# Kernel optimization log

Hardware: AMD Instinct MI355X
Metric: run time of the kernel (lower is better)

The kernel has to match this reference:

```python
import jax, jax.numpy as jnp
import numpy as np

B, S, D, H, L, K = 16, 384, 512, 8, 4, 7
HD = D // H
MAXLEN = 400


def _pos_encoding(d=D, max_len=MAXLEN):
    # Faithful to the (unusual) torch loop: even idx i -> sin(pos/10000**(2i/d)),
    # odd idx i+1 -> cos(pos/10000**(2(i+1)/d))
    pe = np.zeros((max_len, d), dtype=np.float32)
    pos = np.arange(max_len, dtype=np.float64)[:, None]
    i = np.arange(0, d, 2)
    pe[:, i] = np.sin(pos / 10000.0 ** (2 * i / d))
    pe[:, i + 1] = np.cos(pos / 10000.0 ** (2 * (i + 1) / d))
    return jnp.asarray(pe)

POS_ENC = _pos_encoding()


def layer_norm(x, g, b, eps=1e-5):
    m = jnp.mean(x, -1, keepdims=True)
    v = jnp.mean((x - m) ** 2, -1, keepdims=True)
    return (x - m) * jax.lax.rsqrt(v + eps) * g + b


def dsconv(x, dw_w, pw_w, pw_b):
    # x: [B,S,D]; depthwise conv1d (no bias) then pointwise 1x1 (bias)
    xc = jnp.transpose(x, (0, 2, 1))  # [B,D,S]
    y = jax.lax.conv_general_dilated(
        xc, dw_w, window_strides=(1,), padding=[(K // 2, K // 2)],
        dimension_numbers=("NCH", "OIH", "NCH"), feature_group_count=D)  # [B,D,S]
    return jnp.einsum("bcs,oc->bso", y, pw_w) + pw_b  # [B,S,D]


def setup_inputs():
    key = jax.random.key(0)
    ks = jax.random.split(key, 16)
    sc = 0.02
    inp = {
        "x": jax.random.normal(ks[0], (B, S, D), jnp.float32),
        "mask": jax.random.randint(ks[1], (B, S), 0, 2, jnp.int32),
        "dw_w": jax.random.normal(ks[2], (L, D, 1, K), jnp.float32) * sc,
        "pw_w": jax.random.normal(ks[3], (L, D, D), jnp.float32) * sc,
        "pw_b": jnp.zeros((L, D), jnp.float32),
        "conv_ln_g": jnp.ones((L, D), jnp.float32),
        "conv_ln_b": jnp.zeros((L, D), jnp.float32),
        "pos_ln_g": jnp.ones((D,), jnp.float32),
        "pos_ln_b": jnp.zeros((D,), jnp.float32),
        "wq": jax.random.normal(ks[4], (D, D), jnp.float32) * sc,
        "bq": jnp.zeros((D,), jnp.float32),
        "wk": jax.random.normal(ks[5], (D, D), jnp.float32) * sc,
        "bk": jnp.zeros((D,), jnp.float32),
        "wv": jax.random.normal(ks[6], (D, D), jnp.float32) * sc,
        "bv": jnp.zeros((D,), jnp.float32),
        "wo": jax.random.normal(ks[7], (D, D), jnp.float32) * sc,
        "bo": jnp.zeros((D,), jnp.float32),
        "ff_ln_g": jnp.ones((D,), jnp.float32),
        "ff_ln_b": jnp.zeros((D,), jnp.float32),
        "ff_w": jax.random.normal(ks[8], (D, D), jnp.float32) * sc,
        "ff_b": jnp.zeros((D,), jnp.float32),
    }
    return inp


def attention(x, mask, wq, bq, wk, bk, wv, bv, wo, bo):
    def heads(w, b):
        y = jnp.einsum("bsd,od->bso", x, w) + b
        return jnp.transpose(y.reshape(B, S, H, HD), (0, 2, 1, 3))  # [B,H,S,HD]
    q, k, v = heads(wq, bq), heads(wk, bk), heads(wv, bv)
    energy = jnp.einsum("bhqd,bhkd->bhqk", q, k) / jnp.sqrt(jnp.float32(HD))
    m = (mask == 1)[:, None, None, :]  # [B,1,1,S]
    energy = jnp.where(m, jnp.float32(-1e10), energy)
    alpha = jax.nn.softmax(energy, axis=-1)  # dropout = identity (eval)
    a = jnp.einsum("bhqk,bhkd->bhqd", alpha, v)
    a = jnp.transpose(a, (0, 2, 1, 3)).reshape(B, S, D)
    return jnp.einsum("bsd,od->bso", a, wo) + bo


def reference(x, mask, dw_w, pw_w, pw_b, conv_ln_g, conv_ln_b, pos_ln_g, pos_ln_b,
              wq, bq, wk, bk, wv, bv, wo, bo, ff_ln_g, ff_ln_b, ff_w, ff_b):
    out = x + POS_ENC[None, :S, :]
    res = out
    out = layer_norm(out, pos_ln_g, pos_ln_b)
    for i in range(L):
        out = jax.nn.relu(dsconv(out, dw_w[i], pw_w[i], pw_b[i]))
        out = out + res  # dropout = identity (eval)
        res = out
        out = layer_norm(out, conv_ln_g[i], conv_ln_b[i])
    out = attention(out, mask, wq, bq, wk, bk, wv, bv, wo, bo)
    out = out + res
    res = out
    out = layer_norm(out, ff_ln_g, ff_ln_b)
    out = jax.nn.relu(jnp.einsum("bsd,od->bso", out, ff_w) + ff_b)
    return out + res
```

## Files before the change

kernel.cpp:

```cpp
#include <hip/hip_runtime.h>

#define BB 16
#define SS 384
#define DD 512
#define HH 8
#define HDIM 64
#define LLAY 4
#define KW 7
#define MM (BB*SS)

typedef unsigned short u16;
typedef unsigned int u32;
typedef short short8v __attribute__((ext_vector_type(8)));
typedef float floatx4 __attribute__((ext_vector_type(4)));

__device__ __forceinline__ float bf2f(u16 u) {
    union { u32 i; float f; } v; v.i = ((u32)u) << 16; return v.f;
}
__device__ __forceinline__ u16 f2bf(float f) {
    union { float f; u32 i; } v; v.f = f;
    return (u16)((v.i + 0x7FFFu + ((v.i >> 16) & 1u)) >> 16);
}
__device__ __forceinline__ bool sniff_f32(const void* dtp) {
    return *((const u32*)dtp) == 0x3F800000u;
}
__device__ __forceinline__ float ldf(const void* p, long i, bool f32) {
    return f32 ? ((const float*)p)[i] : bf2f(((const u16*)p)[i]);
}
__device__ __forceinline__ short8v ldfrag_scalar(const void* p, long i, bool f32) {
    short8v r;
    if (f32) {
        const float* q = (const float*)p + i;
#pragma unroll
        for (int j = 0; j < 8; j++) r[j] = (short)f2bf(q[j]);
    } else {
        r = *(const short8v*)((const u16*)p + i);
    }
    return r;
}

__device__ __forceinline__ void load_lds16(const u16* g, u16* l) {
    __builtin_amdgcn_global_load_lds((const __attribute__((address_space(1))) void*)g,
                                     (__attribute__((address_space(3))) void*)l, 16, 0, 0);
}
__device__ __forceinline__ int swz(int row) { return (row & 3) ^ ((row >> 2) & 3); }
__device__ __forceinline__ short8v lds_frag(const u16* buf, int row, int quad) {
    return *(const short8v*)(buf + ((size_t)row * 4 + (quad ^ swz(row))) * 8);
}

#define WCV_DW 2359296
#define WCV_TOT (WCV_DW + LLAY*KW*DD)
#define NCVB ((WCV_TOT + 255) / 256)

__global__ __launch_bounds__(256) void posln_cvt_kernel(
    const void* __restrict__ x, const void* __restrict__ g, const void* __restrict__ bvec,
    u16* __restrict__ res, u16* __restrict__ out,
    const void* __restrict__ pw_w, const void* __restrict__ wq,
    const void* __restrict__ wk, const void* __restrict__ wv,
    const void* __restrict__ wo, const void* __restrict__ ff_w,
    const void* __restrict__ dw_w, u16* __restrict__ wdst,
    const void* __restrict__ dtp) {
    const bool f32 = sniff_f32(dtp);
    const int tid = threadIdx.x;
    if (blockIdx.x >= MM) {
        const int i = (blockIdx.x - MM) * 256 + tid;
        if (i >= WCV_TOT) return;
        const void* src; long idx;
        if (i < 1048576) { src = pw_w; idx = i; }
        else if (i < WCV_DW) {
            const int j = i - 1048576;
            const int m = j >> 18;
            idx = j & 262143;
            src = (m == 0) ? wq : (m == 1) ? wk : (m == 2) ? wv : (m == 3) ? wo : ff_w;
        } else {
            const int j = i - WCV_DW;
            const int l = j / (KW * DD);
            const int r1 = j % (KW * DD);
            const int t = r1 / DD, c = r1 % DD;
            src = dw_w; idx = ((long)l * DD + c) * KW + t;
        }
        wdst[i] = f2bf(ldf(src, idx, f32));
        return;
    }
    const int row = blockIdx.x;
    const int s = row % SS;
    float v[2];
#pragma unroll
    for (int i = 0; i < 2; i++) {
        const int d = tid + i * 256;
        const float freq = __expf(-(float)d * 0.035977892078032f);
        const float arg = (float)s * freq;
        const float pe = (d & 1) ? __cosf(arg) : __sinf(arg);
        v[i] = ldf(x, (long)row * DD + d, f32) + pe;
        res[row * DD + d] = f2bf(v[i]);
    }
    float sum = v[0] + v[1], sq = v[0] * v[0] + v[1] * v[1];
#pragma unroll
    for (int off = 32; off; off >>= 1) { sum += __shfl_down(sum, off); sq += __shfl_down(sq, off); }
    __shared__ float red[4][2];
    const int wv2 = tid >> 6;
    if ((tid & 63) == 0) { red[wv2][0] = sum; red[wv2][1] = sq; }
    __syncthreads();
    sum = red[0][0] + red[1][0] + red[2][0] + red[3][0];
    sq  = red[0][1] + red[1][1] + red[2][1] + red[3][1];
    const float mean = sum * (1.f / DD);
    const float rstd = rsqrtf(sq * (1.f / DD) - mean * mean + 1e-5f);
#pragma unroll
    for (int i = 0; i < 2; i++) {
        const int d = tid + i * 256;
        out[row * DD + d] = f2bf((v[i] - mean) * rstd * ldf(g, d, f32) + ldf(bvec, d, f32));
    }
}

template <int VEC>
__global__ __launch_bounds__(256) void dwconv_kernel(const u16* __restrict__ in,
                                                     const void* __restrict__ w, int layer,
                                                     u16* __restrict__ out,
                                                     const void* __restrict__ dtp) {
    if constexpr (VEC) {
        const int bsw = (blockIdx.x & 7) * (MM * DD / 8 / 256 / 8) + (blockIdx.x >> 3);
        const int idx = bsw * 256 + threadIdx.x;
        const int c8 = (idx & 63) * 8;
        const int ms = idx >> 6;
        const int s = ms % SS;
        const u16* wl = (const u16*)w + (size_t)layer * KW * DD;
        float acc[8] = {0, 0, 0, 0, 0, 0, 0, 0};
#pragma unroll
        for (int t = 0; t < KW; t++) {
            const int ss2 = s + t - 3;
            if (ss2 >= 0 && ss2 < SS) {
                const short8v iv = *(const short8v*)(in + (size_t)(ms + t - 3) * DD + c8);
                const short8v wv = *(const short8v*)(wl + t * DD + c8);
#pragma unroll
                for (int j = 0; j < 8; j++)
                    acc[j] += bf2f((u16)iv[j]) * bf2f((u16)wv[j]);
            }
        }
        short8v ov;
#pragma unroll
        for (int j = 0; j < 8; j++) ov[j] = (short)f2bf(acc[j]);
        *(short8v*)(out + (size_t)ms * DD + c8) = ov;
    } else {
        const bool f32 = sniff_f32(dtp);
        const long woff = (long)layer * DD * KW;
        const int idx = blockIdx.x * 256 + threadIdx.x;
        const int c = idx & (DD - 1);
        const int ms = idx >> 9;
        const int s = ms % SS;
        float acc = 0.f;
#pragma unroll
        for (int t = 0; t < KW; t++) {
            const int ss2 = s + t - 3;
            if (ss2 >= 0 && ss2 < SS)
                acc += bf2f(in[(ms + t - 3) * DD + c]) * ldf(w, woff + c * KW + t, f32);
        }
        out[idx] = f2bf(acc);
    }
}

__device__ __forceinline__ void stage_tile16(const u16* A, const u16* W, int m0,
                                             u16* Abuf, u16* Wbuf, int tid, int k0) {
#pragma unroll
    for (int j = 0; j < 4; j++) {
        const int c = j * 512 + tid;
        const int row = c >> 2;
        const int kpart = (c & 3) ^ swz(row);
        load_lds16(W + (size_t)row * DD + k0 + kpart * 8, Wbuf + (size_t)c * 8);
    }
    if (tid < 64) {
        const int row = tid >> 2;
        const int kpart = (tid & 3) ^ swz(row);
        load_lds16(A + (size_t)(m0 + row) * DD + k0 + kpart * 8, Abuf + (size_t)tid * 8);
    }
}

__device__ __forceinline__ void kloop16(const u16* A, const u16* W, int m0,
                                        u16* Abuf, u16* Wbuf,
                                        int tid, int wave, int ln15, int quad,
                                        floatx4 acc[4]) {
    stage_tile16(A, W, m0, Abuf, Wbuf, tid, 0);
    __syncthreads();
    for (int ks = 0; ks < 16; ks++) {
        const int cur = ks & 1;
        u16* Ab = Abuf + cur * (16 * 32);
        u16* Wb = Wbuf + cur * (DD * 32);
        if (ks < 15)
            stage_tile16(A, W, m0, Abuf + (cur ^ 1) * (16 * 32),
                         Wbuf + (cur ^ 1) * (DD * 32), tid, (ks + 1) * 32);
        const short8v a0 = lds_frag(Ab, ln15, quad);
#pragma unroll
        for (int nt = 0; nt < 4; nt++) {
            const short8v b = lds_frag(Wb, wave * 64 + nt * 16 + ln15, quad);
            acc[nt] = __builtin_amdgcn_mfma_f32_16x16x32_bf16(a0, b, acc[nt], 0, 0, 0);
        }
        __syncthreads();
    }
}

template <int RELU, int DO_LN, int FINAL, int WVEC>
__global__ __launch_bounds__(512, 4) void gemm16_kernel(
    const u16* __restrict__ A, const void* __restrict__ W, int wlayer,
    const void* __restrict__ bias, const void* __restrict__ g,
    const void* __restrict__ bvec, int blayer,
    const u16* __restrict__ res_in, u16* __restrict__ res_out,
    void* __restrict__ out, const void* __restrict__ dtp) {
    const bool f32 = sniff_f32(dtp);
    const long woff = (long)wlayer * DD * DD;
    const long voff = (long)blayer * DD;
    __shared__ float part[8][16][2];
    __shared__ __align__(16) u16 Wbuf[2 * DD * 32];
    __shared__ __align__(16) u16 Abuf[2 * 16 * 32];
    const int tid = threadIdx.x;
    const int m0 = blockIdx.x * 16;
    const int wave = tid >> 6, lane = tid & 63;
    const int ln15 = lane & 15, quad = lane >> 4;

    floatx4 acc[4];
#pragma unroll
    for (int nt = 0; nt < 4; nt++) acc[nt] = {0.f, 0.f, 0.f, 0.f};

    if constexpr (WVEC) {
        kloop16(A, (const u16*)W + woff, m0, Abuf, Wbuf, tid, wave, ln15, quad, acc);
    } else {
        const u16* A0 = A + (size_t)(m0 + ln15) * DD + quad * 8;
#pragma unroll
        for (int ks = 0; ks < 16; ks++) {
            const int k0 = ks * 32;
            short8v a0 = *(const short8v*)(A0 + k0);
            short8v b[4];
#pragma unroll
            for (int nt = 0; nt < 4; nt++) {
                const long wrow = woff + (long)(wave * 64 + nt * 16 + ln15) * DD + quad * 8 + k0;
                b[nt] = ldfrag_scalar(W, wrow, f32);
            }
#pragma unroll
            for (int nt = 0; nt < 4; nt++)
                acc[nt] = __builtin_amdgcn_mfma_f32_16x16x32_bf16(a0, b[nt], acc[nt], 0, 0, 0);
        }
    }

#pragma unroll
    for (int nt = 0; nt < 4; nt++) {
        const int col = wave * 64 + nt * 16 + ln15;
        const float bval = ldf(bias, voff + col, f32);
#pragma unroll
        for (int r = 0; r < 4; r++) {
            const int m = m0 + quad * 4 + r;
            float y = acc[nt][r] + bval;
            if (RELU) y = fmaxf(y, 0.f);
            y += bf2f(res_in[(size_t)m * DD + col]);
            if (res_out) res_out[(size_t)m * DD + col] = f2bf(y);
            acc[nt][r] = y;
        }
    }
    if constexpr (DO_LN) {
        float ls[4], lq[4];
#pragma unroll
        for (int r = 0; r < 4; r++) {
            float s = 0.f, q = 0.f;
#pragma unroll
            for (int nt = 0; nt < 4; nt++) { const float y = acc[nt][r]; s += y; q += y * y; }
            ls[r] = s; lq[r] = q;
        }
#pragma unroll
        for (int off = 1; off < 16; off <<= 1)
#pragma unroll
            for (int r = 0; r < 4; r++) {
                ls[r] += __shfl_xor(ls[r], off);
                lq[r] += __shfl_xor(lq[r], off);
            }
        if (ln15 == 0) {
#pragma unroll
            for (int r = 0; r < 4; r++) {
                part[wave][quad * 4 + r][0] = ls[r];
                part[wave][quad * 4 + r][1] = lq[r];
            }
        }
        __syncthreads();
        float mean[4], rstd[4];
#pragma unroll
        for (int r = 0; r < 4; r++) {
            const int rr = quad * 4 + r;
            float s = 0.f, q = 0.f;
#pragma unroll
            for (int wv = 0; wv < 8; wv++) { s += part[wv][rr][0]; q += part[wv][rr][1]; }
            const float mn = s * (1.f / DD);
            mean[r] = mn;
            rstd[r] = rsqrtf(q * (1.f / DD) - mn * mn + 1e-5f);
        }
#pragma unroll
        for (int nt = 0; nt < 4; nt++) {
            const int col = wave * 64 + nt * 16 + ln15;
            const float gv = ldf(g, voff + col, f32);
            const float bv = ldf(bvec, voff + col, f32);
#pragma unroll
            for (int r = 0; r < 4; r++) {
                const int m = m0 + quad * 4 + r;
                ((u16*)out)[(size_t)m * DD + col] =
                    f2bf((acc[nt][r] - mean[r]) * rstd[r] * gv + bv);
            }
        }
    } else {
#pragma unroll
        for (int nt = 0; nt < 4; nt++) {
            const int col = wave * 64 + nt * 16 + ln15;
#pragma unroll
            for (int r = 0; r < 4; r++) {
                const int m = m0 + quad * 4 + r;
                if (FINAL && f32) ((float*)out)[(size_t)m * DD + col] = acc[nt][r];
                else              ((u16*)out)[(size_t)m * DD + col] = f2bf(acc[nt][r]);
            }
        }
    }
}

#define VPAD 40
template <int WVEC>
__global__ __launch_bounds__(512, 4) void qkv16_kernel(
    const u16* __restrict__ A,
    const void* __restrict__ Wq, const void* __restrict__ Wk, const void* __restrict__ Wv,
    const void* __restrict__ bq, const void* __restrict__ bk, const void* __restrict__ bv,
    u16* __restrict__ qo, u16* __restrict__ ko, u16* __restrict__ vo,
    const void* __restrict__ dtp) {
    const bool f32 = sniff_f32(dtp);
    const int sel = blockIdx.y;
    const void* W = (sel == 0) ? Wq : (sel == 1) ? Wk : Wv;
    const void* bias = (sel == 0) ? bq : (sel == 1) ? bk : bv;
    u16* out = (sel == 0) ? qo : (sel == 1) ? ko : vo;

    __shared__ __align__(16) u16 Wbuf[2 * DD * 32];
    __shared__ __align__(16) u16 Abuf[2 * 16 * 32];
    u16 (*vtile)[64][VPAD] = (u16 (*)[64][VPAD])Wbuf;

    const int tid = threadIdx.x;
    const int m0 = blockIdx.x * 16;
    const int wave = tid >> 6, lane = tid & 63;
    const int ln15 = lane & 15, quad = lane >> 4;
    const int bidx = m0 / SS;

    floatx4 acc[4];
#pragma unroll
    for (int nt = 0; nt < 4; nt++) acc[nt] = {0.f, 0.f, 0.f, 0.f};

    if constexpr (WVEC) {
        kloop16(A, (const u16*)W, m0, Abuf, Wbuf, tid, wave, ln15, quad, acc);
    } else {
        const u16* A0 = A + (size_t)(m0 + ln15) * DD + quad * 8;
#pragma unroll
        for (int ks = 0; ks < 16; ks++) {
            const int k0 = ks * 32;
            short8v a0 = *(const short8v*)(A0 + k0);
            short8v b[4];
#pragma unroll
            for (int nt = 0; nt < 4; nt++) {
                const long wrow = (long)(wave * 64 + nt * 16 + ln15) * DD + quad * 8 + k0;
                b[nt] = ldfrag_scalar(W, wrow, f32);
            }
#pragma unroll
            for (int nt = 0; nt < 4; nt++)
                acc[nt] = __builtin_amdgcn_mfma_f32_16x16x32_bf16(a0, b[nt], acc[nt], 0, 0, 0);
        }
    }

    if (sel == 2) {
#pragma unroll
        for (int nt = 0; nt < 4; nt++) {
            const int c = nt * 16 + ln15;
            const float bval = ldf(bias, wave * 64 + c, f32);
#pragma unroll
            for (int r = 0; r < 4; r++)
                vtile[wave][c][quad * 4 + r] = f2bf(acc[nt][r] + bval);
        }
        __builtin_amdgcn_s_waitcnt(0);
        {
            const int c = lane;
            const int col = wave * 64 + c;
            const int h = col >> 6, hd = col & 63;
            u16* dst = vo + ((size_t)(bidx * HH + h) * HDIM + hd) * SS + (m0 - bidx * SS);
            const u16* srcl = &vtile[wave][c][0];
#pragma unroll
            for (int j = 0; j < 2; j++)
                *(short8v*)(dst + j * 8) = *(const short8v*)(srcl + j * 8);
        }
    } else {
#pragma unroll
        for (int nt = 0; nt < 4; nt++) {
            const int col = wave * 64 + nt * 16 + ln15;
            const int h = col >> 6, hd = col & 63;
            const float bval = ldf(bias, col, f32);
#pragma unroll
            for (int r = 0; r < 4; r++) {
                const int m = m0 + quad * 4 + r;
                const int s = m - bidx * SS;
                out[((size_t)(bidx * HH + h) * SS + s) * HDIM + hd] = f2bf(acc[nt][r] + bval);
            }
        }
    }
}

#define SSPF 388
#define SSPH 392
__global__ __launch_bounds__(256) void attn_kernel(const u16* __restrict__ q,
                                                   const u16* __restrict__ k,
                                                   const u16* __restrict__ vT,
                                                   const int* __restrict__ mask,
                                                   u16* __restrict__ out) {
    __shared__ float sc[16 * SSPF];
    __shared__ float rsum[16];
    u16* al = (u16*)sc;

    const int n = blockIdx.x;
    const int i = n >> 3;
    const int g = (n & 7) * 16 + i / 24;
    const int qt = i % 24;
    const int h = g & 7, b = g >> 3;
    const int q0 = qt * 16;
    const int wave = threadIdx.x >> 6, lane = threadIdx.x & 63;
    const int ln15 = lane & 15, quad = lane >> 4;

    const u16* qh = q + (size_t)(b * HH + h) * SS * HDIM;
    const u16* kh = k + (size_t)(b * HH + h) * SS * HDIM;

    const short8v* arow = (const short8v*)(qh + (q0 + ln15) * HDIM + quad * 8);
    const short8v a0 = arow[0], a1 = arow[4];
#pragma unroll
    for (int t = 0; t < 6; t++) {
        const int n0 = wave * 96 + t * 16;
        const short8v* brow = (const short8v*)(kh + (n0 + ln15) * HDIM + quad * 8);
        floatx4 acc = {0.f, 0.f, 0.f, 0.f};
        __builtin_amdgcn_s_setprio(1);
        acc = __builtin_amdgcn_mfma_f32_16x16x32_bf16(a0, brow[0], acc, 0, 0, 0);
        acc = __builtin_amdgcn_mfma_f32_16x16x32_bf16(a1, brow[4], acc, 0, 0, 0);
        __builtin_amdgcn_s_setprio(0);
        const int kk = n0 + ln15;
        const bool msk = (mask[b * SS + kk] == 1);
#pragma unroll
        for (int r = 0; r < 4; r++) {
            float v = acc[r] * 0.125f;
            if (msk) v = -1e10f;
            sc[(quad * 4 + r) * SSPF + kk] = v;
        }
    }
    __syncthreads();
    const int r = threadIdx.x >> 4, cg = threadIdx.x & 15;
    float pv[24], mx = -3.0e38f;
#pragma unroll
    for (int j = 0; j < 24; j++) { pv[j] = sc[r * SSPF + cg + 16 * j]; mx = fmaxf(mx, pv[j]); }
#pragma unroll
    for (int off = 8; off; off >>= 1) mx = fmaxf(mx, __shfl_xor(mx, off, 16));
    float sum = 0.f;
#pragma unroll
    for (int j = 0; j < 24; j++) { const float p = __expf(pv[j] - mx); pv[j] = p; sum += p; }
#pragma unroll
    for (int off = 8; off; off >>= 1) sum += __shfl_xor(sum, off, 16);
    if (cg == 0) rsum[r] = sum;
    __syncthreads();
#pragma unroll
    for (int j = 0; j < 24; j++) al[r * SSPH + cg + 16 * j] = f2bf(pv[j]);
    __syncthreads();
    const u16* vh = vT + (size_t)(b * HH + h) * HDIM * SS;
    const int d0 = wave * 16;
    floatx4 acc = {0.f, 0.f, 0.f, 0.f};
    __builtin_amdgcn_s_setprio(1);
#pragma unroll
    for (int k0 = 0; k0 < SS; k0 += 32) {
        const short8v af = *(const short8v*)(al + ln15 * SSPH + k0 + quad * 8);
        const short8v bf = *(const short8v*)(vh + (d0 + ln15) * SS + k0 + quad * 8);
        acc = __builtin_amdgcn_mfma_f32_16x16x32_bf16(af, bf, acc, 0, 0, 0);
    }
    __builtin_amdgcn_s_setprio(0);
#pragma unroll
    for (int rr = 0; rr < 4; rr++) {
        const int lr = quad * 4 + rr;
        const int s = q0 + lr;
        out[((size_t)(b * SS + s)) * DD + h * HDIM + d0 + ln15] = f2bf(acc[rr] / rsum[lr]);
    }
}

extern "C" void kernel_launch(void* const* d_in, const int* in_sizes, int n_in,
                              void* d_out, int out_size, void* d_ws, size_t ws_size,
                              hipStream_t stream) {
    (void)in_sizes; (void)n_in; (void)out_size;
    const void* x     = d_in[0];
    const int*  mask  = (const int*)d_in[1];
    const void* dw_w  = d_in[2];
    const void* pw_w  = d_in[3];
    const void* pw_b  = d_in[4];
    const void* cln_g = d_in[5];
    const void* cln_b = d_in[6];
    const void* pln_g = d_in[7];
    const void* pln_b = d_in[8];
    const void* wq    = d_in[9];
    const void* bq    = d_in[10];
    const void* wk    = d_in[11];
    const void* bk    = d_in[12];
    const void* wv    = d_in[13];
    const void* bv    = d_in[14];
    const void* wo    = d_in[15];
    const void* bo    = d_in[16];
    const void* fln_g = d_in[17];
    const void* fln_b = d_in[18];
    const void* ff_w  = d_in[19];
    const void* ff_b  = d_in[20];
    const void* dtp   = cln_g;

    const size_t nAct = (size_t)MM * DD;
    char* p = (char*)d_ws;
    u16* res   = (u16*)p; p += nAct * 2;
    u16* lnout = (u16*)p; p += nAct * 2;
    u16* tmp   = (u16*)p; p += nAct * 2;
    u16* vT    = (u16*)p; p += nAct * 2;
    u16* wcv   = (u16*)p;
    u16* kb    = (u16*)d_out;

    const size_t needFast = nAct * 2 * 4 + (size_t)WCV_TOT * 2;
    const bool fast = (ws_size >= needFast);

    if (fast) {
        posln_cvt_kernel<<<MM + NCVB, 256, 0, stream>>>(
            x, pln_g, pln_b, res, lnout,
            pw_w, wq, wk, wv, wo, ff_w, dw_w, wcv, dtp);
        const u16* w_pw = wcv;
        const u16* w_q  = wcv + 1048576;
        const u16* w_k  = wcv + 1310720;
        const u16* w_v  = wcv + 1572864;
        const u16* w_o  = wcv + 1835008;
        const u16* w_ff = wcv + 2097152;
        const u16* w_dw = wcv + WCV_DW;

        for (int i = 0; i < LLAY; i++) {
            dwconv_kernel<1><<<MM * DD / 8 / 256, 256, 0, stream>>>(lnout, w_dw, i, tmp, dtp);
            gemm16_kernel<1, 1, 0, 1><<<MM / 16, 512, 0, stream>>>(
                tmp, w_pw + (size_t)i * DD * DD, 0, pw_b, cln_g, cln_b, i,
                res, res, lnout, dtp);
        }
        qkv16_kernel<1><<<dim3(MM / 16, 3), 512, 0, stream>>>(
            lnout, w_q, w_k, w_v, bq, bk, bv, tmp, kb, vT, dtp);

        attn_kernel<<<BB * HH * (SS / 16), 256, 0, stream>>>(tmp, kb, vT, mask, lnout);

        gemm16_kernel<0, 1, 0, 1><<<MM / 16, 512, 0, stream>>>(
            lnout, w_o, 0, bo, fln_g, fln_b, 0, res, res, lnout, dtp);
        gemm16_kernel<1, 0, 1, 1><<<MM / 16, 512, 0, stream>>>(
            lnout, w_ff, 0, ff_b, nullptr, nullptr, 0, res, nullptr, d_out, dtp);
    } else {
        posln_cvt_kernel<<<MM, 256, 0, stream>>>(
            x, pln_g, pln_b, res, lnout,
            pw_w, wq, wk, wv, wo, ff_w, dw_w, (u16*)d_ws, dtp);
        for (int i = 0; i < LLAY; i++) {
            dwconv_kernel<0><<<MM * DD / 256, 256, 0, stream>>>(lnout, dw_w, i, tmp, dtp);
            gemm16_kernel<1, 1, 0, 0><<<MM / 16, 512, 0, stream>>>(
                tmp, pw_w, i, pw_b, cln_g, cln_b, i, res, res, lnout, dtp);
        }
        qkv16_kernel<0><<<dim3(MM / 16, 3), 512, 0, stream>>>(
            lnout, wq, wk, wv, bq, bk, bv, tmp, kb, vT, dtp);

        attn_kernel<<<BB * HH * (SS / 16), 256, 0, stream>>>(tmp, kb, vT, mask, lnout);

        gemm16_kernel<0, 1, 0, 0><<<MM / 16, 512, 0, stream>>>(
            lnout, wo, 0, bo, fln_g, fln_b, 0, res, res, lnout, dtp);
        gemm16_kernel<1, 0, 1, 0><<<MM / 16, 512, 0, stream>>>(
            lnout, ff_w, 0, ff_b, nullptr, nullptr, 0, res, nullptr, d_out, dtp);
    }
}
```

Baseline: 367.4 us.

## Use 64x128 tiled GEMMs with separate residual LayerNorm kernel

Replaces the 16-row full-width GEMM, which staged the entire 512-column weight slice per 16 rows, with a 64x128 block-tiled GEMM. Each weight tile is now reused across 64 rows, and each block computes 8 MFMA tiles per wave. Because the row-wise LayerNorm can no longer be fused into a GEMM epilogue that spans only 128 columns, a separate lnres kernel is added, which costs an extra read and write of the residual per layer. The QKV projection gets the same tiling, with a transposed V tile written through LDS.

```diff
diff --git a/kernel.cpp b/kernel.cpp
--- a/kernel.cpp
+++ b/kernel.cpp
@@ -12,6 +12,7 @@
 typedef unsigned short u16;
 typedef unsigned int u32;
 typedef short short8v __attribute__((ext_vector_type(8)));
+typedef short short4v __attribute__((ext_vector_type(4)));
 typedef float floatx4 __attribute__((ext_vector_type(4)));
 
 __device__ __forceinline__ float bf2f(u16 u) {
@@ -112,6 +113,33 @@
     }
 }
 
+__global__ __launch_bounds__(512) void lnres_kernel(const u16* __restrict__ y,
+                                                    const void* __restrict__ g,
+                                                    const void* __restrict__ bvec,
+                                                    int blayer,
+                                                    u16* __restrict__ out,
+                                                    const void* __restrict__ dtp) {
+    const bool f32 = sniff_f32(dtp);
+    const long voff = (long)blayer * DD;
+    const int row = blockIdx.x * 8 + (threadIdx.x >> 6);
+    const int lane = threadIdx.x & 63;
+    const short8v v = *(const short8v*)(y + (size_t)row * DD + lane * 8);
+    float f[8], sum = 0.f, sq = 0.f;
+#pragma unroll
+    for (int j = 0; j < 8; j++) { f[j] = bf2f((u16)v[j]); sum += f[j]; sq += f[j] * f[j]; }
+#pragma unroll
+    for (int off = 32; off; off >>= 1) { sum += __shfl_xor(sum, off); sq += __shfl_xor(sq, off); }
+    const float mean = sum * (1.f / DD);
+    const float rstd = rsqrtf(sq * (1.f / DD) - mean * mean + 1e-5f);
+    short8v o;
+#pragma unroll
+    for (int j = 0; j < 8; j++) {
+        const int d = lane * 8 + j;
+        o[j] = (short)f2bf((f[j] - mean) * rstd * ldf(g, voff + d, f32) + ldf(bvec, voff + d, f32));
+    }
+    *(short8v*)(out + (size_t)row * DD + lane * 8) = o;
+}
+
 template <int VEC>
 __global__ __launch_bounds__(256) void dwconv_kernel(const u16* __restrict__ in,
                                                      const void* __restrict__ w, int layer,
@@ -158,46 +186,170 @@
     }
 }
 
-__device__ __forceinline__ void stage_tile16(const u16* A, const u16* W, int m0,
-                                             u16* Abuf, u16* Wbuf, int tid, int k0) {
-#pragma unroll
-    for (int j = 0; j < 4; j++) {
-        const int c = j * 512 + tid;
+__device__ __forceinline__ void stage64(const u16* A, const u16* Wp, int m0,
+                                        u16* Ab, u16* Wb, int tid, int k0) {
+#pragma unroll
+    for (int j = 0; j < 2; j++) {
+        const int c = j * 256 + tid;
         const int row = c >> 2;
-        const int kpart = (c & 3) ^ swz(row);
-        load_lds16(W + (size_t)row * DD + k0 + kpart * 8, Wbuf + (size_t)c * 8);
-    }
-    if (tid < 64) {
+        const int kp = (c & 3) ^ swz(row);
+        load_lds16(Wp + (size_t)row * DD + k0 + kp * 8, Wb + (size_t)c * 8);
+    }
+    {
         const int row = tid >> 2;
-        const int kpart = (tid & 3) ^ swz(row);
-        load_lds16(A + (size_t)(m0 + row) * DD + k0 + kpart * 8, Abuf + (size_t)tid * 8);
-    }
-}
-
-__device__ __forceinline__ void kloop16(const u16* A, const u16* W, int m0,
+        const int kp = (tid & 3) ^ swz(row);
+        load_lds16(A + (size_t)(m0 + row) * DD + k0 + kp * 8, Ab + (size_t)tid * 8);
+    }
+}
+
+__device__ __forceinline__ floatx4 mfma16(short8v a, short8v b, floatx4 c) {
+    return __builtin_amdgcn_mfma_f32_16x16x32_bf16(a, b, c, 0, 0, 0);
+}
+
+__device__ __forceinline__ void kloop64(const u16* A, const u16* Wp, int m0,
                                         u16* Abuf, u16* Wbuf,
-                                        int tid, int wave, int ln15, int quad,
-                                        floatx4 acc[4]) {
-    stage_tile16(A, W, m0, Abuf, Wbuf, tid, 0);
+                                        int tid, int wm, int wn, int ln15, int quad,
+                                        floatx4 acc[2][4]) {
+    stage64(A, Wp, m0, Abuf, Wbuf, tid, 0);
     __syncthreads();
     for (int ks = 0; ks < 16; ks++) {
         const int cur = ks & 1;
-        u16* Ab = Abuf + cur * (16 * 32);
-        u16* Wb = Wbuf + cur * (DD * 32);
+        u16* Ab = Abuf + cur * (64 * 32);
+        u16* Wb = Wbuf + cur * (128 * 32);
         if (ks < 15)
-            stage_tile16(A, W, m0, Abuf + (cur ^ 1) * (16 * 32),
-                         Wbuf + (cur ^ 1) * (DD * 32), tid, (ks + 1) * 32);
-        const short8v a0 = lds_frag(Ab, ln15, quad);
-#pragma unroll
-        for (int nt = 0; nt < 4; nt++) {
-            const short8v b = lds_frag(Wb, wave * 64 + nt * 16 + ln15, quad);
-            acc[nt] = __builtin_amdgcn_mfma_f32_16x16x32_bf16(a0, b, acc[nt], 0, 0, 0);
+            stage64(A, Wp, m0, Abuf + (cur ^ 1) * (64 * 32),
+                    Wbuf + (cur ^ 1) * (128 * 32), tid, (ks + 1) * 32);
+        const short8v a0 = lds_frag(Ab, wm * 32 + ln15, quad);
+        const short8v a1 = lds_frag(Ab, wm * 32 + 16 + ln15, quad);
+#pragma unroll
+        for (int nt = 0; nt < 4; nt++) {
+            const short8v b = lds_frag(Wb, wn * 64 + nt * 16 + ln15, quad);
+            acc[0][nt] = mfma16(a0, b, acc[0][nt]);
+            acc[1][nt] = mfma16(a1, b, acc[1][nt]);
         }
         __syncthreads();
     }
 }
 
-template <int RELU, int DO_LN, int FINAL, int WVEC>
+template <int RELU, int FINAL>
+__global__ __launch_bounds__(256, 4) void gemm64_kernel(
+    const u16* __restrict__ A, const u16* __restrict__ W,
+    const void* __restrict__ bias, int blayer,
+    const u16* __restrict__ res_in, u16* __restrict__ res_out,
+    void* __restrict__ out, const void* __restrict__ dtp) {
+    const bool f32 = sniff_f32(dtp);
+    const long voff = (long)blayer * DD;
+    __shared__ __align__(16) u16 smem[12288];
+    u16* Wbuf = smem;
+    u16* Abuf = smem + 8192;
+    const int tid = threadIdx.x;
+    const int m0 = blockIdx.x * 64, n0 = blockIdx.y * 128;
+    const int wave = tid >> 6, lane = tid & 63;
+    const int wm = wave >> 1, wn = wave & 1;
+    const int ln15 = lane & 15, quad = lane >> 4;
+
+    floatx4 acc[2][4];
+#pragma unroll
+    for (int mt = 0; mt < 2; mt++)
+#pragma unroll
+        for (int nt = 0; nt < 4; nt++) acc[mt][nt] = {0.f, 0.f, 0.f, 0.f};
+
+    kloop64(A, W + (size_t)n0 * DD, m0, Abuf, Wbuf, tid, wm, wn, ln15, quad, acc);
+
+#pragma unroll
+    for (int nt = 0; nt < 4; nt++) {
+        const int col = n0 + wn * 64 + nt * 16 + ln15;
+        const float bval = ldf(bias, voff + col, f32);
+#pragma unroll
+        for (int mt = 0; mt < 2; mt++)
+#pragma unroll
+            for (int r = 0; r < 4; r++) {
+                const int m = m0 + wm * 32 + mt * 16 + quad * 4 + r;
+                float y = acc[mt][nt][r] + bval;
+                if (RELU) y = fmaxf(y, 0.f);
+                y += bf2f(res_in[(size_t)m * DD + col]);
+                if (res_out) res_out[(size_t)m * DD + col] = f2bf(y);
+                if constexpr (FINAL) {
+                    if (f32) ((float*)out)[(size_t)m * DD + col] = y;
+                    else     ((u16*)out)[(size_t)m * DD + col] = f2bf(y);
+                }
+            }
+    }
+}
+
+#define VP 72
+__global__ __launch_bounds__(256, 4) void qkv64_kernel(
+    const u16* __restrict__ A,
+    const u16* __restrict__ Wq, const u16* __restrict__ Wk, const u16* __restrict__ Wv,
+    const void* __restrict__ bq, const void* __restrict__ bk, const void* __restrict__ bv,
+    u16* __restrict__ qo, u16* __restrict__ ko, u16* __restrict__ vo,
+    const void* __restrict__ dtp) {
+    const bool f32 = sniff_f32(dtp);
+    const int sel = blockIdx.z;
+    const u16* W = (sel == 0) ? Wq : (sel == 1) ? Wk : Wv;
+    const void* bias = (sel == 0) ? bq : (sel == 1) ? bk : bv;
+
+    __shared__ __align__(16) u16 smem[12288];
+    u16* Wbuf = smem;
+    u16* Abuf = smem + 8192;
+    u16 (*vtile)[VP] = (u16 (*)[VP])smem;
+
+    const int tid = threadIdx.x;
+    const int m0 = blockIdx.x * 64, n0 = blockIdx.y * 128;
+    const int wave = tid >> 6, lane = tid & 63;
+    const int wm = wave >> 1, wn = wave & 1;
+    const int ln15 = lane & 15, quad = lane >> 4;
+    const int bidx = m0 / SS;
+
+    floatx4 acc[2][4];
+#pragma unroll
+    for (int mt = 0; mt < 2; mt++)
+#pragma unroll
+        for (int nt = 0; nt < 4; nt++) acc[mt][nt] = {0.f, 0.f, 0.f, 0.f};
+
+    kloop64(A, W + (size_t)n0 * DD, m0, Abuf, Wbuf, tid, wm, wn, ln15, quad, acc);
+
+    if (sel == 2) {
+#pragma unroll
+        for (int nt = 0; nt < 4; nt++) {
+            const int cl = wn * 64 + nt * 16 + ln15;
+            const float bval = ldf(bias, n0 + cl, f32);
+#pragma unroll
+            for (int mt = 0; mt < 2; mt++)
+#pragma unroll
+                for (int r = 0; r < 4; r++)
+                    vtile[cl][wm * 32 + mt * 16 + quad * 4 + r] = f2bf(acc[mt][nt][r] + bval);
+        }
+        __syncthreads();
+        const int c = tid & 127, half = tid >> 7;
+        const int col = n0 + c;
+        const int h = col >> 6, hd = col & 63;
+        u16* dst = vo + ((size_t)(bidx * HH + h) * HDIM + hd) * SS
+                      + (m0 - bidx * SS) + half * 32;
+        const u16* srcl = &vtile[c][half * 32];
+#pragma unroll
+        for (int j = 0; j < 4; j++)
+            *(short8v*)(dst + j * 8) = *(const short8v*)(srcl + j * 8);
+    } else {
+        u16* out = (sel == 0) ? qo : ko;
+#pragma unroll
+        for (int nt = 0; nt < 4; nt++) {
+            const int col = n0 + wn * 64 + nt * 16 + ln15;
+            const int h = col >> 6, hd = col & 63;
+            const float bval = ldf(bias, col, f32);
+#pragma unroll
+            for (int mt = 0; mt < 2; mt++)
+#pragma unroll
+                for (int r = 0; r < 4; r++) {
+                    const int m = m0 + wm * 32 + mt * 16 + quad * 4 + r;
+                    const int s = m - bidx * SS;
+                    out[((size_t)(bidx * HH + h) * SS + s) * HDIM + hd] = f2bf(acc[mt][nt][r] + bval);
+                }
+        }
+    }
+}
+
+template <int RELU, int DO_LN, int FINAL>
 __global__ __launch_bounds__(512, 4) void gemm16_kernel(
     const u16* __restrict__ A, const void* __restrict__ W, int wlayer,
     const void* __restrict__ bias, const void* __restrict__ g,
@@ -208,8 +360,6 @@
     const long woff = (long)wlayer * DD * DD;
     const long voff = (long)blayer * DD;
     __shared__ float part[8][16][2];
-    __shared__ __align__(16) u16 Wbuf[2 * DD * 32];
-    __shared__ __align__(16) u16 Abuf[2 * 16 * 32];
     const int tid = threadIdx.x;
     const int m0 = blockIdx.x * 16;
     const int wave = tid >> 6, lane = tid & 63;
@@ -219,24 +369,20 @@
 #pragma unroll
     for (int nt = 0; nt < 4; nt++) acc[nt] = {0.f, 0.f, 0.f, 0.f};
 
-    if constexpr (WVEC) {
-        kloop16(A, (const u16*)W + woff, m0, Abuf, Wbuf, tid, wave, ln15, quad, acc);
-    } else {
-        const u16* A0 = A + (size_t)(m0 + ln15) * DD + quad * 8;
-#pragma unroll
-        for (int ks = 0; ks < 16; ks++) {
-            const int k0 = ks * 32;
-            short8v a0 = *(const short8v*)(A0 + k0);
-            short8v b[4];
-#pragma unroll
-            for (int nt = 0; nt < 4; nt++) {
-                const long wrow = woff + (long)(wave * 64 + nt * 16 + ln15) * DD + quad * 8 + k0;
-                b[nt] = ldfrag_scalar(W, wrow, f32);
-            }
-#pragma unroll
-            for (int nt = 0; nt < 4; nt++)
-                acc[nt] = __builtin_amdgcn_mfma_f32_16x16x32_bf16(a0, b[nt], acc[nt], 0, 0, 0);
-        }
+    const u16* A0 = A + (size_t)(m0 + ln15) * DD + quad * 8;
+#pragma unroll
+    for (int ks = 0; ks < 16; ks++) {
+        const int k0 = ks * 32;
+        short8v a0 = *(const short8v*)(A0 + k0);
+        short8v b[4];
+#pragma unroll
+        for (int nt = 0; nt < 4; nt++) {
+            const long wrow = woff + (long)(wave * 64 + nt * 16 + ln15) * DD + quad * 8 + k0;
+            b[nt] = ldfrag_scalar(W, wrow, f32);
+        }
+#pragma unroll
+        for (int nt = 0; nt < 4; nt++)
+            acc[nt] = mfma16(a0, b[nt], acc[nt]);
     }
 
 #pragma unroll
@@ -314,8 +460,6 @@
     }
 }
 
-#define VPAD 40
-template <int WVEC>
 __global__ __launch_bounds__(512, 4) void qkv16_kernel(
     const u16* __restrict__ A,
     const void* __restrict__ Wq, const void* __restrict__ Wk, const void* __restrict__ Wv,
@@ -326,11 +470,6 @@
     const int sel = blockIdx.y;
     const void* W = (sel == 0) ? Wq : (sel == 1) ? Wk : Wv;
     const void* bias = (sel == 0) ? bq : (sel == 1) ? bk : bv;
-    u16* out = (sel == 0) ? qo : (sel == 1) ? ko : vo;
-
-    __shared__ __align__(16) u16 Wbuf[2 * DD * 32];
-    __shared__ __align__(16) u16 Abuf[2 * 16 * 32];
-    u16 (*vtile)[64][VPAD] = (u16 (*)[64][VPAD])Wbuf;
 
     const int tid = threadIdx.x;
     const int m0 = blockIdx.x * 16;
@@ -342,47 +481,37 @@
 #pragma unroll
     for (int nt = 0; nt < 4; nt++) acc[nt] = {0.f, 0.f, 0.f, 0.f};
 
-    if constexpr (WVEC) {
-        kloop16(A, (const u16*)W, m0, Abuf, Wbuf, tid, wave, ln15, quad, acc);
+    const u16* A0 = A + (size_t)(m0 + ln15) * DD + quad * 8;
+#pragma unroll
+    for (int ks = 0; ks < 16; ks++) {
+        const int k0 = ks * 32;
+        short8v a0 = *(const short8v*)(A0 + k0);
+        short8v b[4];
+#pragma unroll
+        for (int nt = 0; nt < 4; nt++) {
+            const long wrow = (long)(wave * 64 + nt * 16 + ln15) * DD + quad * 8 + k0;
+            b[nt] = ldfrag_scalar(W, wrow, f32);
+        }
+#pragma unroll
+        for (int nt = 0; nt < 4; nt++)
+            acc[nt] = mfma16(a0, b[nt], acc[nt]);
+    }
+
+    if (sel == 2) {
+#pragma unroll
+        for (int nt = 0; nt < 4; nt++) {
+            const int col = wave * 64 + nt * 16 + ln15;
+            const int h = col >> 6, hd = col & 63;
+            const float bval = ldf(bias, col, f32);
+#pragma unroll
+            for (int r = 0; r < 4; r++) {
+                const int m = m0 + quad * 4 + r;
+                const int s = m - bidx * SS;
+                vo[((size_t)(bidx * HH + h) * HDIM + hd) * SS + s] = f2bf(acc[nt][r] + bval);
+            }
+        }
     } else {
-        const u16* A0 = A + (size_t)(m0 + ln15) * DD + quad * 8;
-#pragma unroll
-        for (int ks = 0; ks < 16; ks++) {
-            const int k0 = ks * 32;
-            short8v a0 = *(const short8v*)(A0 + k0);
-            short8v b[4];
-#pragma unroll
-            for (int nt = 0; nt < 4; nt++) {
-                const long wrow = (long)(wave * 64 + nt * 16 + ln15) * DD + quad * 8 + k0;
-                b[nt] = ldfrag_scalar(W, wrow, f32);
-            }
-#pragma unroll
-            for (int nt = 0; nt < 4; nt++)
-                acc[nt] = __builtin_amdgcn_mfma_f32_16x16x32_bf16(a0, b[nt], acc[nt], 0, 0, 0);
-        }
-    }
-
-    if (sel == 2) {
-#pragma unroll
-        for (int nt = 0; nt < 4; nt++) {
-            const int c = nt * 16 + ln15;
-            const float bval = ldf(bias, wave * 64 + c, f32);
-#pragma unroll
-            for (int r = 0; r < 4; r++)
-                vtile[wave][c][quad * 4 + r] = f2bf(acc[nt][r] + bval);
-        }
-        __builtin_amdgcn_s_waitcnt(0);
-        {
-            const int c = lane;
-            const int col = wave * 64 + c;
-            const int h = col >> 6, hd = col & 63;
-            u16* dst = vo + ((size_t)(bidx * HH + h) * HDIM + hd) * SS + (m0 - bidx * SS);
-            const u16* srcl = &vtile[wave][c][0];
-#pragma unroll
-            for (int j = 0; j < 2; j++)
-                *(short8v*)(dst + j * 8) = *(const short8v*)(srcl + j * 8);
-        }
-    } else {
+        u16* out = (sel == 0) ? qo : ko;
 #pragma unroll
         for (int nt = 0; nt < 4; nt++) {
             const int col = wave * 64 + nt * 16 + ln15;
@@ -429,8 +558,8 @@
         const short8v* brow = (const short8v*)(kh + (n0 + ln15) * HDIM + quad * 8);
         floatx4 acc = {0.f, 0.f, 0.f, 0.f};
         __builtin_amdgcn_s_setprio(1);
-        acc = __builtin_amdgcn_mfma_f32_16x16x32_bf16(a0, brow[0], acc, 0, 0, 0);
-        acc = __builtin_amdgcn_mfma_f32_16x16x32_bf16(a1, brow[4], acc, 0, 0, 0);
+        acc = mfma16(a0, brow[0], acc);
+        acc = mfma16(a1, brow[4], acc);
         __builtin_amdgcn_s_setprio(0);
         const int kk = n0 + ln15;
         const bool msk = (mask[b * SS + kk] == 1);
@@ -466,7 +595,7 @@
     for (int k0 = 0; k0 < SS; k0 += 32) {
         const short8v af = *(const short8v*)(al + ln15 * SSPH + k0 + quad * 8);
         const short8v bf = *(const short8v*)(vh + (d0 + ln15) * SS + k0 + quad * 8);
-        acc = __builtin_amdgcn_mfma_f32_16x16x32_bf16(af, bf, acc, 0, 0, 0);
+        acc = mfma16(af, bf, acc);
     }
     __builtin_amdgcn_s_setprio(0);
 #pragma unroll
@@ -530,36 +659,37 @@
 
         for (int i = 0; i < LLAY; i++) {
             dwconv_kernel<1><<<MM * DD / 8 / 256, 256, 0, stream>>>(lnout, w_dw, i, tmp, dtp);
-            gemm16_kernel<1, 1, 0, 1><<<MM / 16, 512, 0, stream>>>(
-                tmp, w_pw + (size_t)i * DD * DD, 0, pw_b, cln_g, cln_b, i,
-                res, res, lnout, dtp);
-        }
-        qkv16_kernel<1><<<dim3(MM / 16, 3), 512, 0, stream>>>(
+            gemm64_kernel<1, 0><<<dim3(MM / 64, 4), 256, 0, stream>>>(
+                tmp, w_pw + (size_t)i * DD * DD, pw_b, i, res, res, nullptr, dtp);
+            lnres_kernel<<<MM / 8, 512, 0, stream>>>(res, cln_g, cln_b, i, lnout, dtp);
+        }
+        qkv64_kernel<<<dim3(MM / 64, 4, 3), 256, 0, stream>>>(
             lnout, w_q, w_k, w_v, bq, bk, bv, tmp, kb, vT, dtp);
 
         attn_kernel<<<BB * HH * (SS / 16), 256, 0, stream>>>(tmp, kb, vT, mask, lnout);
 
-        gemm16_kernel<0, 1, 0, 1><<<MM / 16, 512, 0, stream>>>(
-            lnout, w_o, 0, bo, fln_g, fln_b, 0, res, res, lnout, dtp);
-        gemm16_kernel<1, 0, 1, 1><<<MM / 16, 512, 0, stream>>>(
-            lnout, w_ff, 0, ff_b, nullptr, nullptr, 0, res, nullptr, d_out, dtp);
+        gemm64_kernel<0, 0><<<dim3(MM / 64, 4), 256, 0, stream>>>(
+            lnout, w_o, bo, 0, res, res, nullptr, dtp);
+        lnres_kernel<<<MM / 8, 512, 0, stream>>>(res, fln_g, fln_b, 0, lnout, dtp);
+        gemm64_kernel<1, 1><<<dim3(MM / 64, 4), 256, 0, stream>>>(
+            lnout, w_ff, ff_b, 0, res, nullptr, d_out, dtp);
     } else {
         posln_cvt_kernel<<<MM, 256, 0, stream>>>(
             x, pln_g, pln_b, res, lnout,
             pw_w, wq, wk, wv, wo, ff_w, dw_w, (u16*)d_ws, dtp);
         for (int i = 0; i < LLAY; i++) {
             dwconv_kernel<0><<<MM * DD / 256, 256, 0, stream>>>(lnout, dw_w, i, tmp, dtp);
-            gemm16_kernel<1, 1, 0, 0><<<MM / 16, 512, 0, stream>>>(
+            gemm16_kernel<1, 1, 0><<<MM / 16, 512, 0, stream>>>(
                 tmp, pw_w, i, pw_b, cln_g, cln_b, i, res, res, lnout, dtp);
         }
-        qkv16_kernel<0><<<dim3(MM / 16, 3), 512, 0, stream>>>(
+        qkv16_kernel<<<dim3(MM / 16, 3), 512, 0, stream>>>(
             lnout, wq, wk, wv, bq, bk, bv, tmp, kb, vT, dtp);
 
         attn_kernel<<<BB * HH * (SS / 16), 256, 0, stream>>>(tmp, kb, vT, mask, lnout);
 
-        gemm16_kernel<0, 1, 0, 0><<<MM / 16, 512, 0, stream>>>(
+        gemm16_kernel<0, 1, 0><<<MM / 16, 512, 0, stream>>>(
             lnout, wo, 0, bo, fln_g, fln_b, 0, res, res, lnout, dtp);
-        gemm16_kernel<1, 0, 1, 0><<<MM / 16, 512, 0, stream>>>(
+        gemm16_kernel<1, 0, 1><<<MM / 16, 512, 0, stream>>>(
             lnout, ff_w, 0, ff_b, nullptr, nullptr, 0, res, nullptr, d_out, dtp);
     }
 }
```

Result: faster. 349.4 us (-4.9%).
